# Kernel optimization log

Measured on AMD Instinct MI355X. Metric: run time of the kernel, lower is better.

## Reference

```python
import jax, jax.numpy as jnp
import numpy as np

NUM_TOKENS = 16384
MODEL_DIM = 4096
MAX_EXPERTS = 128
INITIAL_EXPERTS = 64
THRESHOLD = 0.5  # rm_threshold


def setup_inputs() -> dict:
    key = jax.random.key(0)
    k1, k2 = jax.random.split(key)
    x = jax.random.normal(k1, (NUM_TOKENS, MODEL_DIM), dtype=jnp.float32)
    # Linear(model_dim, max_expert_num, bias=False).weight -> [E_max, D]
    wg_weight = jax.random.normal(k2, (MAX_EXPERTS, MODEL_DIM), dtype=jnp.float32) * (1.0 / np.sqrt(MODEL_DIM))
    # experts_mask: first `INITIAL_EXPERTS` active
    experts_mask = (jnp.arange(MAX_EXPERTS) < INITIAL_EXPERTS).astype(jnp.float32)
    return {"x": x, "wg_weight": wg_weight, "experts_mask": experts_mask}


def reference(x, wg_weight, experts_mask):
    # gate logits: [N, E_max]
    scores = jnp.einsum("nd,ed->ne", x, wg_weight)
    # mask inactive experts
    scores = jnp.where(experts_mask[None, :] == 0, jnp.float32(-1e9), scores)
    # fp32 softmax + epsilon (matches F.softmax(..., dtype=float32) + 1e-14)
    scores = jax.nn.softmax(scores.astype(jnp.float32), axis=-1) + 1e-14
    # sort descending along expert dim
    sorted_scores = -jnp.sort(-scores, axis=-1)
    cum_scores = jnp.cumsum(sorted_scores, axis=-1)
    # adaptive top-k: experts needed to accumulate THRESHOLD routing mass
    mask = (cum_scores - sorted_scores) < THRESHOLD
    top_k = mask.sum(axis=-1).astype(jnp.int32)
    active_experts = experts_mask.sum().astype(jnp.int32)
    top_k = jnp.minimum(top_k, active_experts)
    return scores.astype(x.dtype), top_k
```

## Files before the change

kernel.cpp:

```cpp
#include <hip/hip_runtime.h>
#include <hip/hip_bf16.h>
#include <stdint.h>

#define NTOK 16384
#define DDIM 4096
#define NEXP 128
#define BM 32
#define BK 64
#define NT (DDIM / BK)

typedef __attribute__((ext_vector_type(8))) short short8;
typedef __attribute__((ext_vector_type(4))) float f32x4;
typedef __attribute__((address_space(1))) const uint32_t gu32;
typedef __attribute__((address_space(3))) uint32_t lu32;

__device__ __forceinline__ void gload16(const void* g, void* l) {
    __builtin_amdgcn_global_load_lds((gu32*)g, (lu32*)l, 16, 0, 0);
}

__device__ __forceinline__ void split_bf16(float f, uint32_t& h, uint32_t& l) {
    uint32_t u = __float_as_uint(f);
    h = (u + 0x7FFFu + ((u >> 16) & 1u)) >> 16;
    float r = f - __uint_as_float(h << 16);
    uint32_t v = __float_as_uint(r);
    l = (v + 0x7FFFu + ((v >> 16) & 1u)) >> 16;
}

__global__ void prep_w(const float* __restrict__ w,
                       uint16_t* __restrict__ whi, uint16_t* __restrict__ wlo) {
    int i = (blockIdx.x * blockDim.x + threadIdx.x) * 4;
    float4 f = *(const float4*)(w + i);
    uint32_t h0, h1, h2, h3, l0, l1, l2, l3;
    split_bf16(f.x, h0, l0);
    split_bf16(f.y, h1, l1);
    split_bf16(f.z, h2, l2);
    split_bf16(f.w, h3, l3);
    uint2 hv = make_uint2(h0 | (h1 << 16), h2 | (h3 << 16));
    uint2 lv = make_uint2(l0 | (l1 << 16), l2 | (l3 << 16));
    *(uint2*)(whi + i) = hv;
    *(uint2*)(wlo + i) = lv;
}

__global__ __launch_bounds__(256) void gemm_logits(
    const float* __restrict__ x,
    const uint16_t* __restrict__ whi, const uint16_t* __restrict__ wlo,
    float* __restrict__ S)
{
    __shared__ uint16_t sAh[2][BM * BK], sAl[2][BM * BK];
    __shared__ uint16_t sBh[2][NEXP * BK], sBl[2][NEXP * BK];

    const int tid  = threadIdx.x;
    const int lane = tid & 63;
    const int wave = tid >> 6;
    const int q = lane >> 4;
    const int c = lane & 15;
    const int rxor = c & 7;
    const int m0 = blockIdx.x * BM;

    const int ar = tid >> 3, aj = tid & 7;
    const float* xp = x + (size_t)(m0 + ar) * DDIM + aj * 8;
    const int aoff = ar * BK + (aj ^ (ar & 7)) * 8;

    const int bjj = aj ^ (ar & 7);
    const size_t bgo = (size_t)ar * DDIM + bjj * 8;
    const int bd = tid * 8;

    f32x4 acc[2][2];
    #pragma unroll
    for (int mt = 0; mt < 2; ++mt)
        #pragma unroll
        for (int nt = 0; nt < 2; ++nt)
            acc[mt][nt] = (f32x4){0.f, 0.f, 0.f, 0.f};

    auto stageB = [&](int nxt, int kn) {
        #pragma unroll
        for (int rr = 0; rr < 4; ++rr) {
            const size_t go = bgo + (size_t)rr * 32 * DDIM + kn;
            gload16(whi + go, &sBh[nxt][bd + rr * 2048]);
            gload16(wlo + go, &sBl[nxt][bd + rr * 2048]);
        }
    };

    auto writeA = [&](int nxt, float4 fa, float4 fb) {
        uint32_t h[8], l[8];
        split_bf16(fa.x, h[0], l[0]); split_bf16(fa.y, h[1], l[1]);
        split_bf16(fa.z, h[2], l[2]); split_bf16(fa.w, h[3], l[3]);
        split_bf16(fb.x, h[4], l[4]); split_bf16(fb.y, h[5], l[5]);
        split_bf16(fb.z, h[6], l[6]); split_bf16(fb.w, h[7], l[7]);
        uint4 hv = make_uint4(h[0] | (h[1] << 16), h[2] | (h[3] << 16),
                              h[4] | (h[5] << 16), h[6] | (h[7] << 16));
        uint4 lv = make_uint4(l[0] | (l[1] << 16), l[2] | (l[3] << 16),
                              l[4] | (l[5] << 16), l[6] | (l[7] << 16));
        *(uint4*)&sAh[nxt][aoff] = hv;
        *(uint4*)&sAl[nxt][aoff] = lv;
    };

    auto compute = [&](int cur) {
        #pragma unroll
        for (int ks = 0; ks < 2; ++ks) {
            const int off = (((ks << 2) | q) ^ rxor) << 3;
            short8 ah[2], alo[2], bh[2], blo[2];
            #pragma unroll
            for (int mt = 0; mt < 2; ++mt) {
                const int ro = (mt * 16 + c) * BK + off;
                ah[mt]  = *(const short8*)&sAh[cur][ro];
                alo[mt] = *(const short8*)&sAl[cur][ro];
            }
            #pragma unroll
            for (int nt = 0; nt < 2; ++nt) {
                const int ro = (wave * 32 + nt * 16 + c) * BK + off;
                bh[nt]  = *(const short8*)&sBh[cur][ro];
                blo[nt] = *(const short8*)&sBl[cur][ro];
            }
            #pragma unroll
            for (int mt = 0; mt < 2; ++mt)
                #pragma unroll
                for (int nt = 0; nt < 2; ++nt) {
                    acc[mt][nt] = __builtin_amdgcn_mfma_f32_16x16x32_bf16(alo[mt], bh[nt],  acc[mt][nt], 0, 0, 0);
                    acc[mt][nt] = __builtin_amdgcn_mfma_f32_16x16x32_bf16(ah[mt],  blo[nt], acc[mt][nt], 0, 0, 0);
                    acc[mt][nt] = __builtin_amdgcn_mfma_f32_16x16x32_bf16(ah[mt],  bh[nt],  acc[mt][nt], 0, 0, 0);
                }
        }
    };

    stageB(0, 0);
    {
        float4 fa = *(const float4*)(xp);
        float4 fb = *(const float4*)(xp + 4);
        writeA(0, fa, fb);
    }
    __syncthreads();

    #pragma unroll 2
    for (int t = 0; t < NT - 1; ++t) {
        const int cur = t & 1, nxt = cur ^ 1;
        const int kn = (t + 1) * BK;
        stageB(nxt, kn);
        float4 fa = *(const float4*)(xp + kn);
        float4 fb = *(const float4*)(xp + kn + 4);
        compute(cur);
        writeA(nxt, fa, fb);
        __syncthreads();
    }
    compute((NT - 1) & 1);

    #pragma unroll
    for (int mt = 0; mt < 2; ++mt)
        #pragma unroll
        for (int nt = 0; nt < 2; ++nt) {
            const int e = wave * 32 + nt * 16 + c;
            #pragma unroll
            for (int r = 0; r < 4; ++r) {
                const int tok = m0 + mt * 16 + q * 4 + r;
                S[(size_t)tok * NEXP + e] = acc[mt][nt][r];
            }
        }
}

__global__ __launch_bounds__(256) void postproc(
    float* __restrict__ S, const float* __restrict__ mask,
    float* __restrict__ topk_out)
{
    const int lane = threadIdx.x & 63;
    const int wave = threadIdx.x >> 6;
    const int g  = lane >> 4;
    const int gl = lane & 15;
    const int tok = blockIdx.x * 16 + wave * 4 + g;
    float* row = S + (size_t)tok * NEXP;

    float v[8];
    bool act[8];
    int cnt = 0;
    #pragma unroll
    for (int j = 0; j < 8; ++j) {
        v[j] = row[gl + 16 * j];
        act[j] = (mask[gl + 16 * j] != 0.f);
        cnt += act[j] ? 1 : 0;
    }
    int active = cnt;
    #pragma unroll
    for (int off = 8; off; off >>= 1) active += __shfl_xor(active, off);

    float mx = -3.0e38f;
    #pragma unroll
    for (int j = 0; j < 8; ++j) mx = fmaxf(mx, act[j] ? v[j] : -3.0e38f);
    #pragma unroll
    for (int off = 8; off; off >>= 1) mx = fmaxf(mx, __shfl_xor(mx, off));

    float sum = 0.f;
    #pragma unroll
    for (int j = 0; j < 8; ++j) {
        v[j] = act[j] ? __expf(v[j] - mx) : 0.f;
        sum += v[j];
    }
    #pragma unroll
    for (int off = 8; off; off >>= 1) sum += __shfl_xor(sum, off);

    const float inv = 1.0f / sum;
    #pragma unroll
    for (int j = 0; j < 8; ++j) {
        v[j] = v[j] * inv + 1e-14f;
        row[gl + 16 * j] = v[j];
    }

    float cum = 0.f;
    int k = 0;
    bool done = false;
    while (__ballot(!done)) {
        if (!done) {
            float mv = v[0];
            #pragma unroll
            for (int j = 1; j < 8; ++j) mv = fmaxf(mv, v[j]);
            #pragma unroll
            for (int off = 8; off; off >>= 1) mv = fmaxf(mv, __shfl_xor(mv, off));
            cum += mv;
            ++k;
            bool has = false;
            #pragma unroll
            for (int j = 0; j < 8; ++j) has |= (v[j] == mv);
            unsigned int m16 = (unsigned int)((__ballot(has) >> (g * 16)) & 0xFFFFull);
            int first = __ffs(m16) - 1;
            if (gl == first) {
                bool cleared = false;
                #pragma unroll
                for (int j = 0; j < 8; ++j) {
                    if (!cleared && v[j] == mv) { v[j] = -1.f; cleared = true; }
                }
            }
            done = (cum >= 0.5f) || (k >= NEXP);
        }
    }
    int topk = k < active ? k : active;
    if (gl == 0) topk_out[tok] = (float)topk;
}

extern "C" void kernel_launch(void* const* d_in, const int* in_sizes, int n_in,
                              void* d_out, int out_size, void* d_ws, size_t ws_size,
                              hipStream_t stream) {
    (void)in_sizes; (void)n_in; (void)out_size; (void)ws_size;
    const float* x    = (const float*)d_in[0];
    const float* w    = (const float*)d_in[1];
    const float* mask = (const float*)d_in[2];

    float* S    = (float*)d_out;
    float* topk = S + (size_t)NTOK * NEXP;

    uint16_t* whi = (uint16_t*)d_ws;
    uint16_t* wlo = whi + (size_t)NEXP * DDIM;

    hipLaunchKernelGGL(prep_w, dim3((NEXP * DDIM) / (256 * 4)), dim3(256), 0, stream,
                       w, whi, wlo);
    hipLaunchKernelGGL(gemm_logits, dim3(NTOK / BM), dim3(256), 0, stream,
                       x, whi, wlo, S);
    hipLaunchKernelGGL(postproc, dim3(NTOK / 16), dim3(256), 0, stream,
                       S, mask, topk);
}
```

Before: 425.8 us.

## Remap B staging per wave, use manual waitcnt barriers, vectorize postproc top-k

In the GEMM, each wave now stages only the B rows it consumes, and __syncthreads is replaced by explicit s_waitcnt/s_barrier with a partial vmcnt wait so global loads can overlap compute. The postproc kernel switches to 8 lanes per token with 16 contiguous float4-loaded values each. Its data-dependent ballot loop becomes a fixed 33-iteration argmax loop using 64-bit key shuffles. The hand-written waitcnt counts are fragile, and the fixed iteration cap assumes top-k never exceeds 33.

```diff
diff --git a/kernel.cpp b/kernel.cpp
--- a/kernel.cpp
+++ b/kernel.cpp
@@ -61,9 +61,10 @@
     const float* xp = x + (size_t)(m0 + ar) * DDIM + aj * 8;
     const int aoff = ar * BK + (aj ^ (ar & 7)) * 8;
 
-    const int bjj = aj ^ (ar & 7);
-    const size_t bgo = (size_t)ar * DDIM + bjj * 8;
-    const int bd = tid * 8;
+    const int brow = wave * 32 + (lane >> 3);
+    const int bjj  = (lane & 7) ^ ((lane >> 3) & 7);
+    const size_t bsrc = (size_t)brow * DDIM + bjj * 8;
+    const int bdst = (wave * 32) * BK + lane * 8;
 
     f32x4 acc[2][2];
     #pragma unroll
@@ -74,10 +75,9 @@
 
     auto stageB = [&](int nxt, int kn) {
         #pragma unroll
-        for (int rr = 0; rr < 4; ++rr) {
-            const size_t go = bgo + (size_t)rr * 32 * DDIM + kn;
-            gload16(whi + go, &sBh[nxt][bd + rr * 2048]);
-            gload16(wlo + go, &sBl[nxt][bd + rr * 2048]);
+        for (int i = 0; i < 4; ++i) {
+            gload16(whi + bsrc + (size_t)(i * 8) * DDIM + kn, &sBh[nxt][bdst + i * 8 * BK]);
+            gload16(wlo + bsrc + (size_t)(i * 8) * DDIM + kn, &sBl[nxt][bdst + i * 8 * BK]);
         }
     };
 
@@ -123,25 +123,31 @@
         }
     };
 
-    stageB(0, 0);
     {
         float4 fa = *(const float4*)(xp);
         float4 fb = *(const float4*)(xp + 4);
+        asm volatile("" ::: "memory");
+        stageB(0, 0);
         writeA(0, fa, fb);
-    }
-    __syncthreads();
+        asm volatile("s_waitcnt vmcnt(0) lgkmcnt(0)" ::: "memory");
+        __builtin_amdgcn_s_barrier();
+    }
 
     #pragma unroll 2
     for (int t = 0; t < NT - 1; ++t) {
         const int cur = t & 1, nxt = cur ^ 1;
         const int kn = (t + 1) * BK;
-        stageB(nxt, kn);
         float4 fa = *(const float4*)(xp + kn);
         float4 fb = *(const float4*)(xp + kn + 4);
+        asm volatile("" ::: "memory");
+        stageB(nxt, kn);
+        asm volatile("s_waitcnt vmcnt(10)" ::: "memory");
         compute(cur);
         writeA(nxt, fa, fb);
-        __syncthreads();
-    }
+        asm volatile("s_waitcnt lgkmcnt(0)" ::: "memory");
+        __builtin_amdgcn_s_barrier();
+    }
+    asm volatile("s_waitcnt vmcnt(0)" ::: "memory");
     compute((NT - 1) & 1);
 
     #pragma unroll
@@ -163,72 +169,74 @@
 {
     const int lane = threadIdx.x & 63;
     const int wave = threadIdx.x >> 6;
-    const int g  = lane >> 4;
-    const int gl = lane & 15;
-    const int tok = blockIdx.x * 16 + wave * 4 + g;
-    float* row = S + (size_t)tok * NEXP;
-
-    float v[8];
-    bool act[8];
+    const int g  = lane >> 3;
+    const int gl = lane & 7;
+    const int tok = blockIdx.x * 32 + wave * 8 + g;
+    float* row = S + (size_t)tok * NEXP + gl * 16;
+    const float* mrow = mask + gl * 16;
+
+    float v[16];
+    #pragma unroll
+    for (int i = 0; i < 4; ++i)
+        *(float4*)&v[i * 4] = *(const float4*)&row[i * 4];
+
+    bool act[16];
     int cnt = 0;
-    #pragma unroll
-    for (int j = 0; j < 8; ++j) {
-        v[j] = row[gl + 16 * j];
-        act[j] = (mask[gl + 16 * j] != 0.f);
+    float mx = -3.0e38f;
+    #pragma unroll
+    for (int j = 0; j < 16; ++j) {
+        act[j] = (mrow[j] != 0.f);
         cnt += act[j] ? 1 : 0;
+        mx = fmaxf(mx, act[j] ? v[j] : -3.0e38f);
     }
     int active = cnt;
     #pragma unroll
-    for (int off = 8; off; off >>= 1) active += __shfl_xor(active, off);
-
-    float mx = -3.0e38f;
-    #pragma unroll
-    for (int j = 0; j < 8; ++j) mx = fmaxf(mx, act[j] ? v[j] : -3.0e38f);
-    #pragma unroll
-    for (int off = 8; off; off >>= 1) mx = fmaxf(mx, __shfl_xor(mx, off));
+    for (int off = 4; off; off >>= 1) active += __shfl_xor(active, off);
+    #pragma unroll
+    for (int off = 4; off; off >>= 1) mx = fmaxf(mx, __shfl_xor(mx, off));
 
     float sum = 0.f;
     #pragma unroll
-    for (int j = 0; j < 8; ++j) {
+    for (int j = 0; j < 16; ++j) {
         v[j] = act[j] ? __expf(v[j] - mx) : 0.f;
         sum += v[j];
     }
     #pragma unroll
-    for (int off = 8; off; off >>= 1) sum += __shfl_xor(sum, off);
+    for (int off = 4; off; off >>= 1) sum += __shfl_xor(sum, off);
 
     const float inv = 1.0f / sum;
     #pragma unroll
-    for (int j = 0; j < 8; ++j) {
-        v[j] = v[j] * inv + 1e-14f;
-        row[gl + 16 * j] = v[j];
-    }
+    for (int j = 0; j < 16; ++j) v[j] = v[j] * inv + 1e-14f;
+    #pragma unroll
+    for (int i = 0; i < 4; ++i)
+        *(float4*)&row[i * 4] = *(const float4*)&v[i * 4];
 
     float cum = 0.f;
     int k = 0;
-    bool done = false;
-    while (__ballot(!done)) {
-        if (!done) {
-            float mv = v[0];
-            #pragma unroll
-            for (int j = 1; j < 8; ++j) mv = fmaxf(mv, v[j]);
-            #pragma unroll
-            for (int off = 8; off; off >>= 1) mv = fmaxf(mv, __shfl_xor(mv, off));
-            cum += mv;
-            ++k;
-            bool has = false;
-            #pragma unroll
-            for (int j = 0; j < 8; ++j) has |= (v[j] == mv);
-            unsigned int m16 = (unsigned int)((__ballot(has) >> (g * 16)) & 0xFFFFull);
-            int first = __ffs(m16) - 1;
-            if (gl == first) {
-                bool cleared = false;
-                #pragma unroll
-                for (int j = 0; j < 8; ++j) {
-                    if (!cleared && v[j] == mv) { v[j] = -1.f; cleared = true; }
-                }
-            }
-            done = (cum >= 0.5f) || (k >= NEXP);
-        }
+    const int base = gl * 16;
+    for (int it = 0; it < 33; ++it) {
+        float lm = v[0];
+        int lj = 0;
+        #pragma unroll
+        for (int j = 1; j < 16; ++j) {
+            const bool gt = v[j] > lm;
+            lm = gt ? v[j] : lm;
+            lj = gt ? j : lj;
+        }
+        unsigned long long key =
+            ((unsigned long long)__float_as_uint(lm) << 32) | (unsigned)(base + lj);
+        #pragma unroll
+        for (int off = 4; off; off >>= 1) {
+            unsigned long long o = __shfl_xor(key, off);
+            key = (o > key) ? o : key;
+        }
+        const float mv = __uint_as_float((uint32_t)(key >> 32));
+        const int widx = (int)(key & 127u);
+        k += (cum < 0.5f) ? 1 : 0;
+        cum += mv;
+        #pragma unroll
+        for (int j = 0; j < 16; ++j)
+            v[j] = (widx == base + j) ? 0.f : v[j];
     }
     int topk = k < active ? k : active;
     if (gl == 0) topk_out[tok] = (float)topk;
@@ -252,6 +260,6 @@
                        w, whi, wlo);
     hipLaunchKernelGGL(gemm_logits, dim3(NTOK / BM), dim3(256), 0, stream,
                        x, whi, wlo, S);
-    hipLaunchKernelGGL(postproc, dim3(NTOK / 16), dim3(256), 0, stream,
+    hipLaunchKernelGGL(postproc, dim3(NTOK / 32), dim3(256), 0, stream,
                        S, mask, topk);
 }
```

After: 477.3 us. 12.1% more time.
